# Kernel tuning notes

Measured on AMD Instinct MI355X. Metric: run time of the kernel, lower is better.

The kernel has to match this reference:

```python
import jax, jax.numpy as jnp
import numpy as np

N_HEADS = 16
NEG_INF = -1e30


def setup_inputs() -> dict:
    key = jax.random.key(0)
    ks = jax.random.split(key, 5)
    B, S, D = 2, 2048, 2048
    scale_w = 1.0 / np.sqrt(D)  # keep activations well-scaled
    return {
        "x": jax.random.normal(ks[0], (B, S, D), dtype=jnp.float32),
        "Wq": jax.random.normal(ks[1], (D, D), dtype=jnp.float32) * scale_w,
        "Wk": jax.random.normal(ks[2], (D, D), dtype=jnp.float32) * scale_w,
        "Wv": jax.random.normal(ks[3], (D, D), dtype=jnp.float32) * scale_w,
        "Wo": jax.random.normal(ks[4], (D, D), dtype=jnp.float32) * scale_w,
    }


def reference(x, Wq, Wk, Wv, Wo):
    # Blocked flash attention with online softmax is exactly causal softmax
    # attention; express it directly.
    B, S, D = x.shape
    H = N_HEADS
    dk = D // H
    scale = 1.0 / np.sqrt(dk)

    def heads(w):
        return (x @ w).reshape(B, S, H, dk)

    q = heads(Wq)  # [B,S,H,dk]
    k = heads(Wk)
    v = heads(Wv)

    scores = jnp.einsum("bqhd,bkhd->bhqk", q, k) * scale  # [B,H,S,S]
    causal = jnp.tril(jnp.ones((S, S), dtype=bool))
    scores = jnp.where(causal, scores, NEG_INF)
    p = jax.nn.softmax(scores, axis=-1)
    o = jnp.einsum("bhqk,bkhd->bqhd", p, v).reshape(B, S, D)
    return o @ Wo
```

## Files before the change

kernel.cpp:

```cpp
#include <hip/hip_runtime.h>
#include <hip/hip_bf16.h>

typedef short s16x8 __attribute__((ext_vector_type(8)));
typedef float f32x4 __attribute__((ext_vector_type(4)));
typedef unsigned short u16x4 __attribute__((ext_vector_type(4)));

#define MFMA16(a, b, c) __builtin_amdgcn_mfma_f32_16x16x32_bf16((a), (b), (c), 0, 0, 0)

__device__ __forceinline__ unsigned short f32_to_bf16(float f) {
  unsigned int u = __builtin_bit_cast(unsigned int, f);
  u += 0x7FFFu + ((u >> 16) & 1u);
  return (unsigned short)(u >> 16);
}

__device__ __forceinline__ void glds16(const unsigned short* g, unsigned short* l) {
  __builtin_amdgcn_global_load_lds(
      (const __attribute__((address_space(1))) void*)g,
      (__attribute__((address_space(3))) void*)l, 16, 0, 0);
}

__global__ void cvt_bf16_k(const float* __restrict__ in, unsigned short* __restrict__ out, int n4) {
  int i = blockIdx.x * 256 + threadIdx.x;
  if (i >= n4) return;
  float4 f = ((const float4*)in)[i];
  u16x4 o;
  o.x = f32_to_bf16(f.x); o.y = f32_to_bf16(f.y);
  o.z = f32_to_bf16(f.z); o.w = f32_to_bf16(f.w);
  ((u16x4*)out)[i] = o;
}

__global__ void cvt_t4_k(const float* __restrict__ Wq, const float* __restrict__ Wk,
                         const float* __restrict__ Wv, const float* __restrict__ Wo,
                         unsigned short* __restrict__ outQKV, unsigned short* __restrict__ outO,
                         int D) {
  int z = blockIdx.z;
  const float* in = (z == 0) ? Wq : (z == 1) ? Wk : (z == 2) ? Wv : Wo;
  unsigned short* out = (z < 3) ? (outQKV + (size_t)z * D * D) : outO;
  __shared__ float tile[32][33];
  int tx = threadIdx.x;
  int nt = D >> 5;
  int bx = blockIdx.x % nt;
  int by = blockIdx.x / nt;
  int r = tx >> 3, c4 = (tx & 7) * 4;
  int k0 = by * 32, n0 = bx * 32;
  float4 f = *(const float4*)(in + (size_t)(k0 + r) * D + n0 + c4);
  tile[r][c4 + 0] = f.x; tile[r][c4 + 1] = f.y;
  tile[r][c4 + 2] = f.z; tile[r][c4 + 3] = f.w;
  __syncthreads();
  u16x4 o;
  o.x = f32_to_bf16(tile[c4 + 0][r]);
  o.y = f32_to_bf16(tile[c4 + 1][r]);
  o.z = f32_to_bf16(tile[c4 + 2][r]);
  o.w = f32_to_bf16(tile[c4 + 3][r]);
  *(u16x4*)(out + (size_t)(n0 + r) * D + k0 + c4) = o;
}

template <int OUTF32>
__global__ __launch_bounds__(512, 2) void gemm3(
    const unsigned short* __restrict__ A, const unsigned short* __restrict__ Bt,
    void* __restrict__ Cv, int M, int N, int K, int ldc) {
  __shared__ unsigned short As[3][256 * 64];
  __shared__ unsigned short Bs[3][128 * 64];
  int t = threadIdx.x, lane = t & 63, w = t >> 6;
  int r16 = lane & 15, kg = lane >> 4;
  int wm = w >> 1, wn = w & 1;
  int nbn = N >> 7;
  int bm = blockIdx.x / nbn, bn = blockIdx.x % nbn;
  const unsigned short* Ag = A + (size_t)bm * 256 * K;
  const unsigned short* Bg = Bt + (size_t)bn * 128 * K;

  const unsigned short* asrc[4];
  const unsigned short* bsrc[2];
  int aoff[4], boff[2];
#pragma unroll
  for (int i = 0; i < 4; ++i) {
    int c = i * 512 + t;
    int row = c >> 3, sl = c & 7;
    asrc[i] = Ag + (size_t)row * K + ((sl ^ (row & 7)) * 8);
    aoff[i] = (i * 512 + (t & ~63)) * 8;
  }
#pragma unroll
  for (int i = 0; i < 2; ++i) {
    int c = i * 512 + t;
    int row = c >> 3, sl = c & 7;
    bsrc[i] = Bg + (size_t)row * K + ((sl ^ (row & 7)) * 8);
    boff[i] = (i * 512 + (t & ~63)) * 8;
  }

  auto STAGE = [&](int bi, int kt2) {
    int k0 = kt2 * 64;
#pragma unroll
    for (int i = 0; i < 4; ++i) glds16(asrc[i] + k0, &As[bi][aoff[i]]);
#pragma unroll
    for (int i = 0; i < 2; ++i) glds16(bsrc[i] + k0, &Bs[bi][boff[i]]);
  };

  f32x4 acc[4][4] = {};
  int nt = K >> 6;
  STAGE(0, 0);
  if (nt > 1) STAGE(1, 1);
  int cur = 0;
  for (int kt = 0; kt < nt; ++kt) {
    if (kt + 1 < nt) {
      asm volatile("s_waitcnt vmcnt(6)" ::: "memory");
    } else {
      asm volatile("s_waitcnt vmcnt(0)" ::: "memory");
    }
    __builtin_amdgcn_s_barrier();
    asm volatile("" ::: "memory");
    if (kt + 2 < nt) {
      int s2 = cur + 2; if (s2 >= 3) s2 -= 3;
      STAGE(s2, kt + 2);
    }
    const unsigned short* Al = As[cur];
    s16x8 af[4][2], bfr[4][2];
#pragma unroll
    for (int mf = 0; mf < 4; ++mf) {
      int row = wm * 64 + mf * 16 + r16;
#pragma unroll
      for (int ks = 0; ks < 2; ++ks)
        af[mf][ks] = *(const s16x8*)&Al[row * 64 + (((ks * 4 + kg) ^ (row & 7)) * 8)];
    }
#pragma unroll
    for (int nf = 0; nf < 4; ++nf) {
      int row = wn * 64 + nf * 16 + r16;
#pragma unroll
      for (int ks = 0; ks < 2; ++ks)
        bfr[nf][ks] = *(const s16x8*)&Bs[cur][row * 64 + (((ks * 4 + kg) ^ (row & 7)) * 8)];
    }
    __builtin_amdgcn_s_setprio(1);
#pragma unroll
    for (int ks = 0; ks < 2; ++ks)
#pragma unroll
      for (int mf = 0; mf < 4; ++mf)
#pragma unroll
        for (int nf = 0; nf < 4; ++nf)
          acc[mf][nf] = MFMA16(af[mf][ks], bfr[nf][ks], acc[mf][nf]);
    __builtin_amdgcn_s_setprio(0);
    cur = (cur == 2) ? 0 : cur + 1;
  }
#pragma unroll
  for (int mf = 0; mf < 4; ++mf)
#pragma unroll
    for (int nf = 0; nf < 4; ++nf)
#pragma unroll
      for (int r = 0; r < 4; ++r) {
        int row = bm * 256 + wm * 64 + mf * 16 + kg * 4 + r;
        int col = bn * 128 + wn * 64 + nf * 16 + r16;
        if (OUTF32)
          ((float*)Cv)[(size_t)row * ldc + col] = acc[mf][nf][r];
        else
          ((unsigned short*)Cv)[(size_t)row * ldc + col] = f32_to_bf16(acc[mf][nf][r]);
      }
}

__global__ __launch_bounds__(256) void vtr_k(const unsigned short* __restrict__ V,
                                             unsigned short* __restrict__ Vt,
                                             int S, int ld) {
  __shared__ unsigned short T[32 * 128];
  int s0 = blockIdx.x * 32, h = blockIdx.y, b = blockIdx.z;
  int H = gridDim.y;
  int t = threadIdx.x;
  const unsigned short* src = V + (size_t)(b * S + s0) * ld + h * 128;
#pragma unroll
  for (int c = 0; c < 2; ++c) {
    int chunk = c * 256 + t;
    int row = chunk >> 4, slot = chunk & 15;
    glds16(src + (size_t)row * ld + slot * 8, &T[(c * 256 + (t & ~63)) * 8]);
  }
  __syncthreads();
  unsigned short* dst = Vt + ((size_t)(b * H + h) * (S >> 3) + (s0 >> 3)) * 1024;
#pragma unroll
  for (int c = 0; c < 2; ++c) {
    int oc = c * 256 + t;
    int sl = oc >> 7, d = oc & 127;
    s16x8 v;
#pragma unroll
    for (int j = 0; j < 8; ++j) v[j] = (short)T[(sl * 8 + j) * 128 + d];
    *(s16x8*)(dst + (size_t)oc * 8) = v;
  }
}

__global__ __launch_bounds__(512) void attn2_k(
    const unsigned short* __restrict__ Q, const unsigned short* __restrict__ Kx,
    const unsigned short* __restrict__ Vt, unsigned short* __restrict__ O,
    int S, int D, int Bn, int ld) {
  const float scale = 0.08838834764831843f;
  int hb = blockIdx.x;
  int h = hb / Bn, b = hb % Bn;
  int NQ = S >> 7;
  int qt = NQ - 1 - blockIdx.y;
  int H = D >> 7;
  int t = threadIdx.x, lane = t & 63, w = t >> 6;
  int r16 = lane & 15, kg = lane >> 4;
  const unsigned short* Qb  = Q + (size_t)b * S * ld + h * 128;
  const unsigned short* Kb  = Kx + (size_t)b * S * ld + h * 128;
  const unsigned short* Vtb = Vt + (size_t)(b * H + h) * (S >> 3) * 1024;

  __shared__ unsigned short Kbuf[2][64 * 128];
  __shared__ unsigned short Vbuf[2][64 * 128];
  __shared__ unsigned short Pl[8][16 * 64];

  auto STAGE = [&](int bufi, int kv0) {
    const unsigned short* Ksrc = Kb + (size_t)kv0 * ld;
#pragma unroll
    for (int c = 0; c < 2; ++c) {
      int chunk = c * 512 + t;
      int row = chunk >> 4, slot = chunk & 15;
      glds16(Ksrc + (size_t)row * ld + ((slot ^ (row & 7)) * 8),
             &Kbuf[bufi][(c * 512 + (t & ~63)) * 8]);
    }
    const unsigned short* Vsrc = Vtb + (size_t)(kv0 >> 3) * 1024;
#pragma unroll
    for (int c = 0; c < 2; ++c) {
      int chunk = c * 512 + t;
      glds16(Vsrc + (size_t)chunk * 8, &Vbuf[bufi][(c * 512 + (t & ~63)) * 8]);
    }
  };

  int W0 = qt * 128 + w * 16;
  int qg = W0 + r16;
  s16x8 qf[4];
#pragma unroll
  for (int ks = 0; ks < 4; ++ks)
    qf[ks] = *(const s16x8*)(Qb + (size_t)qg * ld + ks * 32 + kg * 8);
  f32x4 oacc[8] = {};
  float m_st = -1e30f, l_st = 0.f;
  int nt = (qt + 1) * 2;
  int cur = 0;
  STAGE(0, 0);
  __syncthreads();
  for (int it = 0; it < nt; ++it) {
    int kv0 = it * 64;
    if (it + 1 < nt) STAGE(cur ^ 1, (it + 1) * 64);
    const unsigned short* Kl = Kbuf[cur];
    const unsigned short* Vl = Vbuf[cur];
    if (kv0 <= W0 + 15) {
      f32x4 st4[4];
      __builtin_amdgcn_s_setprio(1);
#pragma unroll
      for (int kf = 0; kf < 4; ++kf) {
        f32x4 s = {};
#pragma unroll
        for (int ks = 0; ks < 4; ++ks) {
          int row = kf * 16 + r16;
          s16x8 kfr = *(const s16x8*)&Kl[row * 128 + (((ks * 4 + kg) ^ (row & 7)) * 8)];
          s = MFMA16(kfr, qf[ks], s);
        }
        st4[kf] = s;
      }
      __builtin_amdgcn_s_setprio(0);
      float p[4][4];
      float mx = -1e30f;
#pragma unroll
      for (int kf = 0; kf < 4; ++kf)
#pragma unroll
        for (int r = 0; r < 4; ++r) {
          int kvg = kv0 + kf * 16 + kg * 4 + r;
          float sv = st4[kf][r] * scale;
          sv = (kvg <= qg) ? sv : -1e30f;
          p[kf][r] = sv;
          mx = fmaxf(mx, sv);
        }
      mx = fmaxf(mx, __shfl_xor(mx, 16, 64));
      mx = fmaxf(mx, __shfl_xor(mx, 32, 64));
      float m_new = fmaxf(m_st, mx);
      float alpha = __expf(m_st - m_new);
      float rs = 0.f;
#pragma unroll
      for (int kf = 0; kf < 4; ++kf)
#pragma unroll
        for (int r = 0; r < 4; ++r) {
          float e = __expf(p[kf][r] - m_new);
          p[kf][r] = e;
          rs += e;
        }
      rs += __shfl_xor(rs, 16, 64);
      rs += __shfl_xor(rs, 32, 64);
      l_st = l_st * alpha + rs;
      m_st = m_new;
#pragma unroll
      for (int kf = 0; kf < 4; ++kf) {
        unsigned int lo = (unsigned int)f32_to_bf16(p[kf][0]) | ((unsigned int)f32_to_bf16(p[kf][1]) << 16);
        unsigned int hi = (unsigned int)f32_to_bf16(p[kf][2]) | ((unsigned int)f32_to_bf16(p[kf][3]) << 16);
        int sslot = 2 * kf + (kg >> 1);
        int base = r16 * 64 + ((sslot ^ (r16 & 7)) * 8) + (kg & 1) * 4;
        *(unsigned int*)&Pl[w][base]     = lo;
        *(unsigned int*)&Pl[w][base + 2] = hi;
      }
      asm volatile("s_waitcnt lgkmcnt(0)" ::: "memory");
      __builtin_amdgcn_sched_barrier(0);
      float ar[4];
#pragma unroll
      for (int r = 0; r < 4; ++r) ar[r] = __shfl(alpha, kg * 4 + r, 64);
#pragma unroll
      for (int f = 0; f < 8; ++f)
#pragma unroll
        for (int r = 0; r < 4; ++r) oacc[f][r] *= ar[r];
      __builtin_amdgcn_s_setprio(1);
#pragma unroll
      for (int tt = 0; tt < 2; ++tt) {
        s16x8 pf = *(const s16x8*)&Pl[w][r16 * 64 + (((4 * tt + kg) ^ (r16 & 7)) * 8)];
#pragma unroll
        for (int f = 0; f < 8; ++f) {
          s16x8 vf = *(const s16x8*)&Vl[((4 * tt + kg) * 128 + f * 16 + r16) * 8];
          oacc[f] = MFMA16(pf, vf, oacc[f]);
        }
      }
      __builtin_amdgcn_s_setprio(0);
    }
    __syncthreads();
    cur ^= 1;
  }
  float linv = 1.0f / l_st;
  float lr[4];
#pragma unroll
  for (int r = 0; r < 4; ++r) lr[r] = __shfl(linv, kg * 4 + r, 64);
#pragma unroll
  for (int f = 0; f < 8; ++f)
#pragma unroll
    for (int r = 0; r < 4; ++r) {
      size_t idx = ((size_t)b * S + W0 + kg * 4 + r) * D + h * 128 + f * 16 + r16;
      O[idx] = f32_to_bf16(oacc[f][r] * lr[r]);
    }
}

extern "C" void kernel_launch(void* const* d_in, const int* in_sizes, int n_in,
                              void* d_out, int out_size, void* d_ws, size_t ws_size,
                              hipStream_t stream) {
  const float* x  = (const float*)d_in[0];
  const float* Wq = (const float*)d_in[1];
  const float* Wk = (const float*)d_in[2];
  const float* Wv = (const float*)d_in[3];
  const float* Wo = (const float*)d_in[4];
  const int D = 2048, H = 16;
  const int M = in_sizes[0] / D;
  const int B = 2, S = M / B;
  const int LD = 3 * D;

  unsigned short* xb    = (unsigned short*)d_ws;
  unsigned short* Wqkvt = xb + (size_t)M * D;
  unsigned short* Wot   = Wqkvt + (size_t)3 * D * D;
  unsigned short* QKVb  = Wot + (size_t)D * D;
  unsigned short* Ob    = xb;
  unsigned short* VtA   = Wqkvt;

  int n4 = M * D / 4;
  cvt_bf16_k<<<(n4 + 255) / 256, 256, 0, stream>>>(x, xb, n4);
  int tgrid = (D / 32) * (D / 32);
  cvt_t4_k<<<dim3(tgrid, 1, 4), 256, 0, stream>>>(Wq, Wk, Wv, Wo, Wqkvt, Wot, D);

  gemm3<0><<<(M / 256) * (LD / 128), 512, 0, stream>>>(xb, Wqkvt, QKVb, M, LD, D, LD);

  vtr_k<<<dim3(S / 32, H, B), 256, 0, stream>>>(QKVb + 2 * D, VtA, S, LD);

  attn2_k<<<dim3(H * B, S / 128), 512, 0, stream>>>(QKVb, QKVb + D, VtA, Ob, S, D, B, LD);

  gemm3<1><<<(M / 256) * (D / 128), 512, 0, stream>>>(Ob, Wot, d_out, M, D, D, D);
}
```

Measured before the change: 297.5 us.

## Rewrite attention with 32x32 MFMA, register-resident P, and conditional rescale

```diff
diff --git a/kernel.cpp b/kernel.cpp
--- a/kernel.cpp
+++ b/kernel.cpp
@@ -3,9 +3,11 @@
 
 typedef short s16x8 __attribute__((ext_vector_type(8)));
 typedef float f32x4 __attribute__((ext_vector_type(4)));
+typedef float f32x16 __attribute__((ext_vector_type(16)));
 typedef unsigned short u16x4 __attribute__((ext_vector_type(4)));
 
 #define MFMA16(a, b, c) __builtin_amdgcn_mfma_f32_16x16x32_bf16((a), (b), (c), 0, 0, 0)
+#define MFMA32(a, b, c) __builtin_amdgcn_mfma_f32_32x32x16_bf16((a), (b), (c), 0, 0, 0)
 
 __device__ __forceinline__ unsigned short f32_to_bf16(float f) {
   unsigned int u = __builtin_bit_cast(unsigned int, f);
@@ -181,7 +183,7 @@
   }
 }
 
-__global__ __launch_bounds__(512) void attn2_k(
+__global__ __launch_bounds__(256) void attn3_k(
     const unsigned short* __restrict__ Q, const unsigned short* __restrict__ Kx,
     const unsigned short* __restrict__ Vt, unsigned short* __restrict__ O,
     int S, int D, int Bn, int ld) {
@@ -192,39 +194,38 @@
   int qt = NQ - 1 - blockIdx.y;
   int H = D >> 7;
   int t = threadIdx.x, lane = t & 63, w = t >> 6;
-  int r16 = lane & 15, kg = lane >> 4;
+  int q31 = lane & 31, hi = lane >> 5;
   const unsigned short* Qb  = Q + (size_t)b * S * ld + h * 128;
   const unsigned short* Kb  = Kx + (size_t)b * S * ld + h * 128;
   const unsigned short* Vtb = Vt + (size_t)(b * H + h) * (S >> 3) * 1024;
 
   __shared__ unsigned short Kbuf[2][64 * 128];
   __shared__ unsigned short Vbuf[2][64 * 128];
-  __shared__ unsigned short Pl[8][16 * 64];
 
   auto STAGE = [&](int bufi, int kv0) {
     const unsigned short* Ksrc = Kb + (size_t)kv0 * ld;
 #pragma unroll
-    for (int c = 0; c < 2; ++c) {
-      int chunk = c * 512 + t;
+    for (int c = 0; c < 4; ++c) {
+      int chunk = c * 256 + t;
       int row = chunk >> 4, slot = chunk & 15;
       glds16(Ksrc + (size_t)row * ld + ((slot ^ (row & 7)) * 8),
-             &Kbuf[bufi][(c * 512 + (t & ~63)) * 8]);
+             &Kbuf[bufi][(c * 256 + (t & ~63)) * 8]);
     }
     const unsigned short* Vsrc = Vtb + (size_t)(kv0 >> 3) * 1024;
 #pragma unroll
-    for (int c = 0; c < 2; ++c) {
-      int chunk = c * 512 + t;
-      glds16(Vsrc + (size_t)chunk * 8, &Vbuf[bufi][(c * 512 + (t & ~63)) * 8]);
+    for (int c = 0; c < 4; ++c) {
+      int chunk = c * 256 + t;
+      glds16(Vsrc + (size_t)chunk * 8, &Vbuf[bufi][(c * 256 + (t & ~63)) * 8]);
     }
   };
 
-  int W0 = qt * 128 + w * 16;
-  int qg = W0 + r16;
-  s16x8 qf[4];
-#pragma unroll
-  for (int ks = 0; ks < 4; ++ks)
-    qf[ks] = *(const s16x8*)(Qb + (size_t)qg * ld + ks * 32 + kg * 8);
-  f32x4 oacc[8] = {};
+  int W0w = qt * 128 + w * 32;
+  int qg = W0w + q31;
+  s16x8 qf[8];
+#pragma unroll
+  for (int ks = 0; ks < 8; ++ks)
+    qf[ks] = *(const s16x8*)(Qb + (size_t)qg * ld + ks * 16 + hi * 8);
+  f32x16 oacc[4] = {};
   float m_st = -1e30f, l_st = 0.f;
   int nt = (qt + 1) * 2;
   int cur = 0;
@@ -235,76 +236,80 @@
     if (it + 1 < nt) STAGE(cur ^ 1, (it + 1) * 64);
     const unsigned short* Kl = Kbuf[cur];
     const unsigned short* Vl = Vbuf[cur];
-    if (kv0 <= W0 + 15) {
-      f32x4 st4[4];
+    if (kv0 <= W0w + 31) {
+      f32x16 st[2] = {};
       __builtin_amdgcn_s_setprio(1);
 #pragma unroll
-      for (int kf = 0; kf < 4; ++kf) {
-        f32x4 s = {};
-#pragma unroll
-        for (int ks = 0; ks < 4; ++ks) {
-          int row = kf * 16 + r16;
-          s16x8 kfr = *(const s16x8*)&Kl[row * 128 + (((ks * 4 + kg) ^ (row & 7)) * 8)];
-          s = MFMA16(kfr, qf[ks], s);
+      for (int kf = 0; kf < 2; ++kf)
+#pragma unroll
+        for (int ks = 0; ks < 8; ++ks) {
+          int row = kf * 32 + q31;
+          s16x8 a = *(const s16x8*)&Kl[row * 128 + (((2 * ks + hi) ^ (row & 7)) * 8)];
+          st[kf] = MFMA32(a, qf[ks], st[kf]);
         }
-        st4[kf] = s;
-      }
       __builtin_amdgcn_s_setprio(0);
-      float p[4][4];
       float mx = -1e30f;
 #pragma unroll
-      for (int kf = 0; kf < 4; ++kf)
-#pragma unroll
-        for (int r = 0; r < 4; ++r) {
-          int kvg = kv0 + kf * 16 + kg * 4 + r;
-          float sv = st4[kf][r] * scale;
+      for (int kf = 0; kf < 2; ++kf)
+#pragma unroll
+        for (int r = 0; r < 16; ++r) {
+          int kvg = kv0 + kf * 32 + (r & 3) + 8 * (r >> 2) + 4 * hi;
+          float sv = st[kf][r] * scale;
           sv = (kvg <= qg) ? sv : -1e30f;
-          p[kf][r] = sv;
+          st[kf][r] = sv;
           mx = fmaxf(mx, sv);
         }
-      mx = fmaxf(mx, __shfl_xor(mx, 16, 64));
       mx = fmaxf(mx, __shfl_xor(mx, 32, 64));
-      float m_new = fmaxf(m_st, mx);
-      float alpha = __expf(m_st - m_new);
+      bool noresc = __all(mx <= m_st);
+      float m_new = noresc ? m_st : fmaxf(m_st, mx);
       float rs = 0.f;
 #pragma unroll
-      for (int kf = 0; kf < 4; ++kf)
-#pragma unroll
-        for (int r = 0; r < 4; ++r) {
-          float e = __expf(p[kf][r] - m_new);
-          p[kf][r] = e;
+      for (int kf = 0; kf < 2; ++kf)
+#pragma unroll
+        for (int r = 0; r < 16; ++r) {
+          float e = __expf(st[kf][r] - m_new);
+          st[kf][r] = e;
           rs += e;
         }
-      rs += __shfl_xor(rs, 16, 64);
       rs += __shfl_xor(rs, 32, 64);
-      l_st = l_st * alpha + rs;
-      m_st = m_new;
-#pragma unroll
-      for (int kf = 0; kf < 4; ++kf) {
-        unsigned int lo = (unsigned int)f32_to_bf16(p[kf][0]) | ((unsigned int)f32_to_bf16(p[kf][1]) << 16);
-        unsigned int hi = (unsigned int)f32_to_bf16(p[kf][2]) | ((unsigned int)f32_to_bf16(p[kf][3]) << 16);
-        int sslot = 2 * kf + (kg >> 1);
-        int base = r16 * 64 + ((sslot ^ (r16 & 7)) * 8) + (kg & 1) * 4;
-        *(unsigned int*)&Pl[w][base]     = lo;
-        *(unsigned int*)&Pl[w][base + 2] = hi;
+      if (!noresc) {
+        float alpha = __expf(m_st - m_new);
+        l_st = l_st * alpha + rs;
+        m_st = m_new;
+#pragma unroll
+        for (int dt = 0; dt < 4; ++dt)
+#pragma unroll
+          for (int r = 0; r < 16; ++r) oacc[dt][r] *= alpha;
+      } else {
+        l_st += rs;
       }
-      asm volatile("s_waitcnt lgkmcnt(0)" ::: "memory");
-      __builtin_amdgcn_sched_barrier(0);
-      float ar[4];
-#pragma unroll
-      for (int r = 0; r < 4; ++r) ar[r] = __shfl(alpha, kg * 4 + r, 64);
-#pragma unroll
-      for (int f = 0; f < 8; ++f)
-#pragma unroll
-        for (int r = 0; r < 4; ++r) oacc[f][r] *= ar[r];
+      unsigned int Dw[2][4][2];
+#pragma unroll
+      for (int kf = 0; kf < 2; ++kf)
+#pragma unroll
+        for (int g = 0; g < 4; ++g)
+#pragma unroll
+          for (int m = 0; m < 2; ++m)
+            Dw[kf][g][m] = (unsigned int)f32_to_bf16(st[kf][4 * g + 2 * m]) |
+                           ((unsigned int)f32_to_bf16(st[kf][4 * g + 2 * m + 1]) << 16);
       __builtin_amdgcn_s_setprio(1);
 #pragma unroll
-      for (int tt = 0; tt < 2; ++tt) {
-        s16x8 pf = *(const s16x8*)&Pl[w][r16 * 64 + (((4 * tt + kg) ^ (r16 & 7)) * 8)];
-#pragma unroll
-        for (int f = 0; f < 8; ++f) {
-          s16x8 vf = *(const s16x8*)&Vl[((4 * tt + kg) * 128 + f * 16 + r16) * 8];
-          oacc[f] = MFMA16(pf, vf, oacc[f]);
+      for (int ks = 0; ks < 4; ++ks) {
+        int kf = ks >> 1, k2 = 2 * (ks & 1);
+        unsigned int L0 = hi ? Dw[kf][k2 + 1][0] : Dw[kf][k2][0];
+        unsigned int L1 = hi ? Dw[kf][k2 + 1][1] : Dw[kf][k2][1];
+        unsigned int Y0 = hi ? Dw[kf][k2][0] : Dw[kf][k2 + 1][0];
+        unsigned int Y1 = hi ? Dw[kf][k2][1] : Dw[kf][k2 + 1][1];
+        unsigned int R0 = __shfl_xor(Y0, 32, 64);
+        unsigned int R1 = __shfl_xor(Y1, 32, 64);
+        uint4 fd;
+        fd.x = hi ? R0 : L0; fd.y = hi ? R1 : L1;
+        fd.z = hi ? L0 : R0; fd.w = hi ? L1 : R1;
+        s16x8 pa = __builtin_bit_cast(s16x8, fd);
+#pragma unroll
+        for (int dt = 0; dt < 4; ++dt) {
+          s16x8 va = *(const s16x8*)&Vl[((2 * ks + hi) * 128 + dt * 32 + q31) * 8];
+          oacc[dt] = MFMA32(va, pa, oacc[dt]);
         }
       }
       __builtin_amdgcn_s_setprio(0);
@@ -313,16 +318,18 @@
     cur ^= 1;
   }
   float linv = 1.0f / l_st;
-  float lr[4];
-#pragma unroll
-  for (int r = 0; r < 4; ++r) lr[r] = __shfl(linv, kg * 4 + r, 64);
-#pragma unroll
-  for (int f = 0; f < 8; ++f)
-#pragma unroll
-    for (int r = 0; r < 4; ++r) {
-      size_t idx = ((size_t)b * S + W0 + kg * 4 + r) * D + h * 128 + f * 16 + r16;
-      O[idx] = f32_to_bf16(oacc[f][r] * lr[r]);
-    }
+  unsigned short* Orow = O + (size_t)(b * S + qg) * D + h * 128;
+#pragma unroll
+  for (int dt = 0; dt < 4; ++dt)
+#pragma unroll
+    for (int g = 0; g < 4; ++g)
+#pragma unroll
+      for (int m = 0; m < 2; ++m) {
+        float o0 = oacc[dt][4 * g + 2 * m] * linv;
+        float o1 = oacc[dt][4 * g + 2 * m + 1] * linv;
+        unsigned int pk = (unsigned int)f32_to_bf16(o0) | ((unsigned int)f32_to_bf16(o1) << 16);
+        *(unsigned int*)(Orow + dt * 32 + 8 * g + 4 * hi + 2 * m) = pk;
+      }
 }
 
 extern "C" void kernel_launch(void* const* d_in, const int* in_sizes, int n_in,
@@ -354,7 +361,7 @@
 
   vtr_k<<<dim3(S / 32, H, B), 256, 0, stream>>>(QKVb + 2 * D, VtA, S, LD);
 
-  attn2_k<<<dim3(H * B, S / 128), 512, 0, stream>>>(QKVb, QKVb + D, VtA, Ob, S, D, B, LD);
+  attn3_k<<<dim3(H * B, S / 128), 256, 0, stream>>>(QKVb, QKVb + D, VtA, Ob, S, D, B, LD);
 
   gemm3<1><<<(M / 256) * (D / 128), 512, 0, stream>>>(Ob, Wot, d_out, M, D, D, D);
 }
```

Measured after the change: 311.0 us. 4.5% more time.
